# Optimization experiments

Measured on AMD Instinct MI355X. Metric: run time of the kernel, lower is better.

Reference implementation:

```python
import jax, jax.numpy as jnp
import numpy as np
from jax import lax

B, PH, PW, D = 4, 256, 256, 128
WS, SS, NG, NH = 8, 4, 2, 4
HID = int(D * 2.0)
DC = D // 2  # ngram-context channel dim


def _window_partition(x, ws):
    b, h, w, c = x.shape
    x = x.reshape(b, h // ws, ws, w // ws, ws, c).transpose(0, 1, 3, 2, 4, 5)
    return x.reshape(-1, ws, ws, c), (h // ws, w // ws)


def _window_unpartition(win, nwin):
    wh, ww = nwin
    _, s1, s2, c = win.shape
    x = win.reshape(-1, wh, ww, s1, s2, c).transpose(0, 1, 3, 2, 4, 5)
    return x.reshape(-1, wh * s1, ww * s2, c)


def _rel_pos_index(wh, ww):
    coords = np.stack(np.meshgrid(np.arange(wh), np.arange(ww), indexing='ij')).reshape(2, -1)
    rel = (coords[:, :, None] - coords[:, None, :]).transpose(1, 2, 0)
    rel[:, :, 0] += wh - 1
    rel[:, :, 1] += ww - 1
    rel[:, :, 0] *= 2 * ww - 1
    return rel.sum(-1)  # [N, N]

RPI_MAIN = jnp.asarray(_rel_pos_index(WS, WS))
RPI_NG = jnp.asarray(_rel_pos_index(NG, NG))


def _layernorm(x, g, b, eps=1e-5):
    mu = x.mean(-1, keepdims=True)
    var = ((x - mu) ** 2).mean(-1, keepdims=True)
    return (x - mu) * lax.rsqrt(var + eps) * g + b


def _mhsa(x, qkv_w, qkv_b, proj_w, proj_b, bias_table, rpi, nheads, mask=None):
    b_, n, c = x.shape
    hd = c // nheads
    qkv = (x @ qkv_w.T + qkv_b).reshape(b_, n, 3, nheads, hd).transpose(2, 0, 3, 1, 4)
    q, k, v = qkv[0] * (hd ** -0.5), qkv[1], qkv[2]
    attn = jnp.einsum('bhnd,bhmd->bhnm', q, k) + bias_table[rpi].transpose(2, 0, 1)[None]
    if mask is not None:
        nw = mask.shape[0]
        attn = (attn.reshape(b_ // nw, nw, nheads, n, n) + mask[None, :, None]).reshape(b_, nheads, n, n)
    attn = jax.nn.softmax(attn, axis=-1)
    out = jnp.einsum('bhnm,bhmd->bhnd', attn, v).transpose(0, 2, 1, 3).reshape(b_, n, c)
    return out @ proj_w.T + proj_b


def _make_mask(ph, pw):
    img = np.zeros((ph, pw), np.float32)
    cnt = 0
    for h in (slice(0, -WS), slice(-WS, -SS), slice(-SS, None)):
        for w in (slice(0, -WS), slice(-WS, -SS), slice(-SS, None)):
            img[h, w] = cnt
            cnt += 1
    mw, _ = _window_partition(jnp.asarray(img)[None, :, :, None], WS)
    mw = mw.reshape(-1, WS * WS)
    diff = mw[:, None, :] - mw[:, :, None]
    return jnp.where(diff != 0, -100.0, 0.0)  # [wh*ww, WS*WS, WS*WS]


def _seq_refl_pad(u, back):
    # sequential reflective window pad by ngram-1 on H and W (front if back else end)
    nh, nw = u.shape[2], u.shape[3]
    if back:
        ih = np.concatenate([np.arange(1, NG), np.arange(nh)])
        iw = np.concatenate([np.arange(1, NG), np.arange(nw)])
    else:
        ih = np.concatenate([np.arange(nh), np.arange(nh - NG, nh - 1)])
        iw = np.concatenate([np.arange(nw), np.arange(nw - NG, nw - 1)])
    return u[:, :, ih][:, :, :, iw]


def _sliding_attn(u, ng_qkv_w, ng_qkv_b, ng_proj_w, ng_proj_b, ng_bias, wh, ww):
    # u: [B, DC, wh+NG-1, ww+NG-1]  (padded unigram)
    hi = (np.arange(wh)[:, None] + np.arange(NG)[None, :]).reshape(-1)
    wi = (np.arange(ww)[:, None] + np.arange(NG)[None, :]).reshape(-1)
    slide = u[:, :, hi][:, :, :, wi].transpose(0, 2, 3, 1)  # [B, wh*NG, ww*NG, DC]
    win, nwin = _window_partition(slide, NG)
    win = win.reshape(-1, NG * NG, DC)
    ctx = _mhsa(win, ng_qkv_w, ng_qkv_b, ng_proj_w, ng_proj_b, ng_bias, RPI_NG, NH)
    ctx = _window_unpartition(ctx.reshape(-1, NG, NG, DC), nwin)  # [B, wh*NG, ww*NG, DC]
    ctx = ctx.transpose(0, 3, 1, 2)
    b = ctx.shape[0]
    return ctx.reshape(b, DC, wh, NG, ww, NG).mean(axis=(3, 5))  # AvgPool2d(NG) -> [B, DC, wh, ww]


def reference(x, uni_w, uni_b, ng_qkv_w, ng_qkv_b, ng_proj_w, ng_proj_b, ng_bias,
              merge_w, merge_b, qkv_w, qkv_b, proj_w, proj_b, bias_table,
              n1_g, n1_b, n2_g, n2_b, fc1_w, fc1_b, fc2_w, fc2_b, ph, pw):
    b = x.shape[0]
    xi = x.reshape(b, ph, pw, D)
    wh, ww = ph // WS, pw // WS
    # --- NGram context ---
    xc = xi.transpose(0, 3, 1, 2)  # NCHW
    uni = lax.conv_general_dilated(xc, uni_w, (WS, WS), 'VALID', feature_group_count=DC,
                                   dimension_numbers=('NCHW', 'OIHW', 'NCHW'))
    uni = uni + uni_b[None, :, None, None]  # [B, DC, wh, ww]
    ctx_f = _sliding_attn(_seq_refl_pad(uni, False), ng_qkv_w, ng_qkv_b, ng_proj_w, ng_proj_b, ng_bias, wh, ww)
    ctx_b = _sliding_attn(_seq_refl_pad(uni, True), ng_qkv_w, ng_qkv_b, ng_proj_w, ng_proj_b, ng_bias, wh, ww)
    ctx = jnp.concatenate([ctx_f, ctx_b], axis=1)  # [B, D, wh, ww]
    ctx = jnp.einsum('bchw,oc->bohw', ctx, merge_w) + merge_b[None, :, None, None]  # 1x1 merge conv
    ctx = ctx.transpose(0, 2, 3, 1)  # [B, wh, ww, D]
    # --- inject context into semi-partitioned windows ---
    windows = xi.reshape(b, wh, WS, ww, WS, D).transpose(0, 1, 3, 2, 4, 5)  # [B, wh, ww, WS, WS, D]
    windows = windows + ctx[:, :, :, None, None, :]
    xw = windows.transpose(0, 1, 3, 2, 4, 5).reshape(b, ph, pw, D)
    # --- cyclic shift + masked window attention ---
    xw = jnp.roll(xw, (-SS, -SS), axis=(1, 2))
    win, _ = _window_partition(xw, WS)
    win = win.reshape(-1, WS * WS, D)
    mask = _make_mask(ph, pw)
    aw = _mhsa(win, qkv_w, qkv_b, proj_w, proj_b, bias_table, RPI_MAIN, NH, mask=mask)
    shifted = _window_unpartition(aw.reshape(-1, WS, WS, D), (wh, ww))  # [B, ph, pw, D]
    rev = jnp.roll(shifted, (SS, SS), axis=(1, 2)).reshape(b, ph * pw, D)
    # --- residual + post-branch layernorm, then FFN ---
    x1 = x + _layernorm(rev, n1_g, n1_b)
    h = jax.nn.gelu(x1 @ fc1_w.T + fc1_b, approximate=False)
    ffn = h @ fc2_w.T + fc2_b
    return x1 + _layernorm(ffn, n2_g, n2_b)


def setup_inputs() -> dict:
    key = jax.random.key(0)
    ks = jax.random.split(key, 12)
    w = lambda k, shape: jax.random.normal(k, shape, jnp.float32) * 0.02
    return {
        'x': jax.random.normal(ks[0], (B, PH * PW, D), jnp.float32),
        'uni_w': w(ks[1], (DC, 2, WS, WS)),
        'uni_b': jnp.zeros((DC,), jnp.float32),
        'ng_qkv_w': w(ks[2], (3 * DC, DC)),
        'ng_qkv_b': jnp.zeros((3 * DC,), jnp.float32),
        'ng_proj_w': w(ks[3], (DC, DC)),
        'ng_proj_b': jnp.zeros((DC,), jnp.float32),
        'ng_bias': w(ks[4], ((2 * NG - 1) ** 2, NH)),
        'merge_w': w(ks[5], (D, D)),
        'merge_b': jnp.zeros((D,), jnp.float32),
        'qkv_w': w(ks[6], (3 * D, D)),
        'qkv_b': jnp.zeros((3 * D,), jnp.float32),
        'proj_w': w(ks[7], (D, D)),
        'proj_b': jnp.zeros((D,), jnp.float32),
        'bias_table': w(ks[8], ((2 * WS - 1) ** 2, NH)),
        'n1_g': jnp.ones((D,), jnp.float32),
        'n1_b': jnp.zeros((D,), jnp.float32),
        'n2_g': jnp.ones((D,), jnp.float32),
        'n2_b': jnp.zeros((D,), jnp.float32),
        'fc1_w': w(ks[9], (HID, D)),
        'fc1_b': jnp.zeros((HID,), jnp.float32),
        'fc2_w': w(ks[10], (D, HID)),
        'fc2_b': jnp.zeros((D,), jnp.float32),
        'ph': PH,
        'pw': PW,
    }
```

## Files before the change

### kernel.cpp

```cpp
#include <hip/hip_runtime.h>

typedef __bf16 bf16x8 __attribute__((ext_vector_type(8)));
typedef __bf16 bf16x4 __attribute__((ext_vector_type(4)));
typedef float  f32x4  __attribute__((ext_vector_type(4)));

#define QSCALE 0.17677669529663687f
#define XF_LD 132

__device__ __forceinline__ f32x4 mfma16(bf16x8 a, bf16x8 b, f32x4 c) {
  return __builtin_amdgcn_mfma_f32_16x16x32_bf16(a, b, c, 0, 0, 0);
}

__device__ __forceinline__ int swz_idx(int row, int col, int rowChunks) {
  return row * (rowChunks << 3) + ((((col >> 3) ^ (row & 7)) << 3) | (col & 7));
}

__device__ __forceinline__ bf16x8 ld_tile(const __bf16* t, int rowChunks,
                                          int rowBase, int chunkBase, int lane) {
  int row = rowBase + (lane & 15);
  int c = (chunkBase + (lane >> 4)) ^ (row & 7);
  return *(const bf16x8*)(t + row * (rowChunks << 3) + (c << 3));
}

__device__ __forceinline__ bf16x8 ld_pack(const __bf16* pk, int nt, int ks,
                                          int ksteps, int lane) {
  int idx = ((nt * ksteps + ks) * 64 + lane) * 8;
  return *(const bf16x8*)(pk + idx);
}

__global__ void k_prep(const float* __restrict__ qkvw, const float* __restrict__ projw,
                       const float* __restrict__ fc1w, const float* __restrict__ fc2w,
                       const float* __restrict__ ngqkvw,
                       const float* __restrict__ ngprojw, const float* __restrict__ ngprojb,
                       const float* __restrict__ mergew, const float* __restrict__ mergeb,
                       const float* __restrict__ bt,
                       const float* __restrict__ x, const float* __restrict__ uw,
                       const float* __restrict__ ub,
                       __bf16* __restrict__ pk, float* __restrict__ w12T,
                       float* __restrict__ fb, float* __restrict__ btf,
                       float* __restrict__ qkvTg, float* __restrict__ uni) {
  int blk = blockIdx.x;
  if (blk < 2048) {
    int bidx = blk * 2 + (threadIdx.x >> 7);
    int b = bidx >> 10, oh = (bidx >> 5) & 31, ow = bidx & 31;
    int d = threadIdx.x & 127;
    const float* xb = x + (((size_t)((b << 16) + ((oh << 3) << 8) + (ow << 3))) << 7) + d;
    const float* w = uw + d * 64;
    float acc = 0.f;
#pragma unroll
    for (int kh = 0; kh < 8; ++kh)
#pragma unroll
      for (int kw = 0; kw < 8; ++kw)
        acc += xb[(size_t)(((kh << 8) + kw)) << 7] * w[kh * 8 + kw];
    acc += __shfl_xor(acc, 1);
    if (!(d & 1)) uni[((size_t)bidx << 6) + (d >> 1)] = acc + ub[d >> 1];
  } else if (blk < 2560) {
    int i = (blk - 2048) * 256 + threadIdx.x;
    const float* src; int K; int e; int scaleQ = 0;
    if (i < 32768)      { src = qkvw;             K = 128; e = i;          scaleQ = 1; }
    else if (i < 49152) { src = qkvw + 256 * 128; K = 128; e = i - 32768; }
    else if (i < 65536) { src = projw;            K = 128; e = i - 49152; }
    else if (i < 98304) { src = fc1w;             K = 128; e = i - 65536; }
    else                { src = fc2w;             K = 256; e = i - 98304; }
    int i8 = e & 7, ln = (e >> 3) & 63, t = e >> 9;
    int ls = (K == 256) ? 3 : 2;
    int ks = t & ((1 << ls) - 1), nt = t >> ls;
    int row = (nt << 4) + (ln & 15);
    int k = (ks << 5) + ((ln >> 4) << 3) + i8;
    float v = src[row * K + k];
    if (scaleQ && row < 128) v *= QSCALE;
    pk[i] = (__bf16)v;
  } else if (blk < 2816) {
    int idx = (blk - 2560) * 256 + threadIdx.x;
    int v = idx >> 14, h = (idx >> 12) & 3, kk = (idx >> 6) & 63, q = idx & 63;
    int s1n = q >> 3, s2n = q & 7, s1m = kk >> 3, s2m = kk & 7;
    int rpi = (s1n - s1m + 7) * 15 + (s2n - s2m + 7);
    float val = bt[rpi * 4 + h];
    if (((v & 1) && ((s1n < 4) != (s1m < 4))) ||
        ((v & 2) && ((s2n < 4) != (s2m < 4))))
      val -= 100.f;
    btf[idx] = val;
  } else if (blk < 2864) {
    int idx = (blk - 2816) * 256 + threadIdx.x;
    int c = idx / 192, o = idx - c * 192;
    qkvTg[idx] = ngqkvw[o * 64 + c] * (o < 64 ? 0.25f : 1.f);
  } else {
    int idx = (blk - 2864) * 256 + threadIdx.x;
    if (idx < 16384) {
      int which = idx >> 13;
      int r = idx & 8191;
      int e = r >> 7, o = r & 127;
      float a = 0.f;
#pragma unroll 8
      for (int d = 0; d < 64; ++d)
        a += mergew[o * 128 + which * 64 + d] * ngprojw[d * 64 + e];
      w12T[idx] = a;
    } else if (idx < 16384 + 128) {
      int o = idx - 16384;
      float a = mergeb[o];
#pragma unroll 8
      for (int d = 0; d < 64; ++d)
        a += (mergew[o * 128 + d] + mergew[o * 128 + 64 + d]) * ngprojb[d];
      fb[o] = a;
    }
  }
}

__global__ void __launch_bounds__(256)
k_ngram(const float* __restrict__ uni, const float* __restrict__ qkvTg,
        const float* __restrict__ ngqkvb, const float* __restrict__ ngbias,
        const float* __restrict__ w12T, const float* __restrict__ fbg,
        float* __restrict__ ctx) {
  extern __shared__ float sm[];
  float* tokl = sm;
  float* qs   = tokl + 2304;
  float* prs  = qs + 6912;
  float* avgl = prs + 256;
  float* ngb  = avgl + 1024;
  float* fbs  = ngb + 192;
  float* nbias= fbs + 128;

  const int t = threadIdx.x;
  const int bidx = blockIdx.x;
  const int b = bidx >> 7, ii = (bidx >> 2) & 31, jq = bidx & 3;
  const int j0 = jq * 8;

  if (t < 192) ngb[t] = ngqkvb[t] * (t < 64 ? 0.25f : 1.f);
  if (t < 128) fbs[t] = fbg[t];
  if (t < 36)  nbias[t] = ngbias[t];
  {
    int w = t >> 6, lane = t & 63;
    int dir = w >> 1, rr = w & 1;
    int pi = ii + rr;
    int srcr = (dir == 0) ? ((pi < 32) ? pi : 30) : ((pi == 0) ? 1 : pi - 1);
#pragma unroll
    for (int cc = 0; cc < 9; ++cc) {
      int pj = j0 + cc;
      int srcc = (dir == 0) ? ((pj < 32) ? pj : 30) : ((pj == 0) ? 1 : pj - 1);
      tokl[((dir * 2 + rr) * 9 + cc) * 64 + lane] =
          uni[(size_t)((b * 32 + srcr) * 32 + srcc) * 64 + lane];
    }
  }
  __syncthreads();

  {
    int w = t >> 6, lane = t & 63;
    for (int itp = 0; itp < 9; ++itp) {
      int pos = itp * 4 + w;
      const float* tk = tokl + pos * 64;
      float a0 = ngb[lane], a1 = ngb[64 + lane], a2 = ngb[128 + lane];
#pragma unroll 4
      for (int c = 0; c < 64; ++c) {
        float tv = tk[c];
        const float* qr = qkvTg + c * 192;
        a0 += qr[lane] * tv;
        a1 += qr[64 + lane] * tv;
        a2 += qr[128 + lane] * tv;
      }
      float* dst = qs + pos * 192;
      dst[lane] = a0; dst[64 + lane] = a1; dst[128 + lane] = a2;
    }
  }
  __syncthreads();

  {
    int dw = t >> 4;
    int idx = t & 15, h = idx >> 2, p = idx & 3;
    int dir = dw >> 3, jl = dw & 7;
    const float* qp = qs + ((dir * 2 + (p >> 1)) * 9 + jl + (p & 1)) * 192 + h * 16;
    float s[4];
#pragma unroll
    for (int m = 0; m < 4; ++m) {
      const float* km = qs + ((dir * 2 + (m >> 1)) * 9 + jl + (m & 1)) * 192 + 64 + h * 16;
      float a = 0.f;
#pragma unroll
      for (int e = 0; e < 16; ++e) a += qp[e] * km[e];
      int bi2 = ((p >> 1) - (m >> 1) + 1) * 3 + ((p & 1) - (m & 1) + 1);
      s[m] = a + nbias[bi2 * 4 + h];
    }
    float mx = fmaxf(fmaxf(s[0], s[1]), fmaxf(s[2], s[3]));
    float e0 = __expf(s[0] - mx), e1 = __expf(s[1] - mx);
    float e2 = __expf(s[2] - mx), e3 = __expf(s[3] - mx);
    float inv = 1.f / (e0 + e1 + e2 + e3);
    float p0 = e0 * inv, p1 = e1 * inv, p2 = e2 * inv, p3 = e3 * inv;
    p0 += __shfl_xor(p0, 1); p0 += __shfl_xor(p0, 2);
    p1 += __shfl_xor(p1, 1); p1 += __shfl_xor(p1, 2);
    p2 += __shfl_xor(p2, 1); p2 += __shfl_xor(p2, 2);
    p3 += __shfl_xor(p3, 1); p3 += __shfl_xor(p3, 2);
    if (p == 0) {
      float* d = prs + (dw * 4 + h) * 4;
      d[0] = p0; d[1] = p1; d[2] = p2; d[3] = p3;
    }
  }
  __syncthreads();

  {
    int w = t >> 6, lane = t & 63;
#pragma unroll
    for (int it = 0; it < 4; ++it) {
      int dw = it * 4 + w;
      int dir = dw >> 3, jl = dw & 7;
      int h = lane >> 4;
      float a = 0.f;
#pragma unroll
      for (int m = 0; m < 4; ++m) {
        float pm = prs[(dw * 4 + h) * 4 + m];
        float vv = qs[((dir * 2 + (m >> 1)) * 9 + jl + (m & 1)) * 192 + 128 + lane];
        a += pm * vv;
      }
      avgl[dw * 64 + lane] = a * 0.25f;
    }
  }
  __syncthreads();

  {
#pragma unroll
    for (int it = 0; it < 4; ++it) {
      int id = it * 256 + t;
      int win = id >> 7, o = id & 127;
      const float* af = avgl + win * 64;
      const float* ab = avgl + (8 + win) * 64;
      float a = fbs[o];
#pragma unroll 4
      for (int c = 0; c < 64; ++c)
        a += w12T[c * 128 + o] * af[c] + w12T[8192 + c * 128 + o] * ab[c];
      int j = j0 + win;
      ctx[((size_t)((b * 32 + ii) * 32 + j)) * 128 + o] = a;
    }
  }
}

__global__ void __launch_bounds__(1024, 2)
k_main(const float* __restrict__ xin, const float* __restrict__ ctx,
       const __bf16* __restrict__ pk_qkv, const __bf16* __restrict__ pk_wv,
       const __bf16* __restrict__ pk_proj, const __bf16* __restrict__ pk_fc1,
       const __bf16* __restrict__ pk_fc2,
       const float* __restrict__ qkvb, const float* __restrict__ projb,
       const float* __restrict__ btf,
       const float* __restrict__ n1g, const float* __restrict__ n1b,
       const float* __restrict__ n2g, const float* __restrict__ n2b,
       const float* __restrict__ fc1b, const float* __restrict__ fc2b,
       float* __restrict__ outp) {
  extern __shared__ char smem[];
  __bf16* Xbf = (__bf16*)smem;
  __bf16* QO  = (__bf16*)(smem + 16 * 1024);
  __bf16* Kl  = (__bf16*)(smem + 32 * 1024);
  __bf16* Vt  = (__bf16*)(smem + 48 * 1024);
  __bf16* Pl  = (__bf16*)(smem + 64 * 1024);
  float*  Rf  = (float*)(smem + 48 * 1024);
  __bf16* Hl  = (__bf16*)(smem + 16 * 1024);
  float*  Ff  = (float*)(smem + 48 * 1024);

  const int widx = blockIdx.x;
  const int b = widx >> 10, wi = (widx >> 5) & 31, wj = widx & 31;
  const int tid = threadIdx.x;
  const int lane = tid & 63, wv = tid >> 6;
  const int lm = lane & 15, lg = lane >> 4;

  float xsv[8];
  float xr[8];

  {
    int n = tid >> 4, c = tid & 15;
    int ts1 = n >> 3, ts2 = n & 7;
    int hh = ((wi << 3) + ts1 + 4) & 255;
    int ww = ((wj << 3) + ts2 + 4) & 255;
    const float* xp = xin + (((size_t)((b << 16) + (hh << 8) + ww)) << 7);
    const float* cp = ctx + (((size_t)((((b << 5) + (hh >> 3)) << 5) + (ww >> 3))) << 7);
    int d0 = c << 2, d1 = 64 + (c << 2);
    float4 x0 = *(const float4*)(xp + d0);
    float4 x1 = *(const float4*)(xp + d1);
    float4 c0 = *(const float4*)(cp + d0);
    float4 c1 = *(const float4*)(cp + d1);
    xsv[0] = x0.x; xsv[1] = x0.y; xsv[2] = x0.z; xsv[3] = x0.w;
    xsv[4] = x1.x; xsv[5] = x1.y; xsv[6] = x1.z; xsv[7] = x1.w;
    bf16x4 pa, pb;
    pa[0] = (__bf16)(x0.x + c0.x); pa[1] = (__bf16)(x0.y + c0.y);
    pa[2] = (__bf16)(x0.z + c0.z); pa[3] = (__bf16)(x0.w + c0.w);
    pb[0] = (__bf16)(x1.x + c1.x); pb[1] = (__bf16)(x1.y + c1.y);
    pb[2] = (__bf16)(x1.z + c1.z); pb[3] = (__bf16)(x1.w + c1.w);
    int cA = d0 >> 3, oA = d0 & 7;
    int cB = d1 >> 3, oB = d1 & 7;
    *(bf16x4*)(Xbf + (n << 7) + (((cA ^ (n & 7)) << 3) | oA)) = pa;
    *(bf16x4*)(Xbf + (n << 7) + (((cB ^ (n & 7)) << 3) | oB)) = pb;
  }
  __syncthreads();

  {
    int ntG = wv;
    bf16x8 wf[4];
#pragma unroll
    for (int ks = 0; ks < 4; ++ks) wf[ks] = ld_pack(pk_qkv, ntG, ks, 4, lane);
    int col0 = (ntG << 4) + (lg << 2);
    float bias[4];
#pragma unroll
    for (int r = 0; r < 4; ++r)
      bias[r] = (ntG < 8) ? qkvb[col0 + r] * QSCALE : qkvb[col0 + r];
    __bf16* dst = (ntG < 8) ? QO : Kl;
    int cc0 = col0 & 127;
    for (int nt = 0; nt < 4; ++nt) {
      bf16x8 xf[4];
#pragma unroll
      for (int ks = 0; ks < 4; ++ks) xf[ks] = ld_tile(Xbf, 16, nt * 16, ks * 4, lane);
      f32x4 acc = {0.f, 0.f, 0.f, 0.f};
#pragma unroll
      for (int ks = 0; ks < 4; ++ks) acc = mfma16(wf[ks], xf[ks], acc);
      int tok = nt * 16 + lm;
      bf16x4 p4;
#pragma unroll
      for (int r = 0; r < 4; ++r) p4[r] = (__bf16)(acc[r] + bias[r]);
      *(bf16x4*)(dst + (tok << 7) + ((((cc0 >> 3) ^ (tok & 7)) << 3) | (cc0 & 7))) = p4;
    }
  }
  {
    int mtG = wv >> 1;
    bf16x8 wvf[4];
#pragma unroll
    for (int ks = 0; ks < 4; ++ks) wvf[ks] = ld_pack(pk_wv, mtG, ks, 4, lane);
    int ch = (mtG << 4) + lm;
    float vb = qkvb[256 + ch];
#pragma unroll
    for (int mt2 = 0; mt2 < 2; ++mt2) {
      int mt = ((wv & 1) << 1) + mt2;
      bf16x8 xf[4];
#pragma unroll
      for (int ks = 0; ks < 4; ++ks) xf[ks] = ld_tile(Xbf, 16, mt * 16, ks * 4, lane);
      f32x4 acc = {0.f, 0.f, 0.f, 0.f};
#pragma unroll
      for (int ks = 0; ks < 4; ++ks) acc = mfma16(xf[ks], wvf[ks], acc);
      int tok0 = mt * 16 + (lg << 2);
      bf16x4 p4;
#pragma unroll
      for (int r = 0; r < 4; ++r) p4[r] = (__bf16)(acc[r] + vb);
      *(bf16x4*)(Vt + (ch << 6) + ((((tok0 >> 3) ^ (ch & 7)) << 3) | (tok0 & 7))) = p4;
    }
  }
  __syncthreads();

  const int h = wv >> 2, mq = wv & 3;
  __bf16* Pme = Pl + (h << 12);
  {
    bf16x8 aq = ld_tile(QO, 16, mq * 16, h * 4, lane);
    bf16x8 bk[4];
#pragma unroll
    for (int nt = 0; nt < 4; ++nt)
      bk[nt] = ld_tile(Kl, 16, nt * 16, h * 4, lane);
    f32x4 sc[4];
#pragma unroll
    for (int nt = 0; nt < 4; ++nt) {
      f32x4 z = {0.f, 0.f, 0.f, 0.f};
      sc[nt] = mfma16(bk[nt], aq, z);
    }
    const int variant = (wi == 31 ? 1 : 0) | (wj == 31 ? 2 : 0);
    const float* btw = btf + (((variant << 2) + h) << 12);
    const int q = mq * 16 + lm;
    float v[4][4];
    float ssum = 0.f;
#pragma unroll
    for (int nt = 0; nt < 4; ++nt)
#pragma unroll
      for (int r = 0; r < 4; ++r) {
        int kk = nt * 16 + (lg << 2) + r;
        float e = __expf(sc[nt][r] + btw[(kk << 6) + q]);
        v[nt][r] = e;
        ssum += e;
      }
    ssum += __shfl_xor(ssum, 16);
    ssum += __shfl_xor(ssum, 32);
    float rinv = 1.f / ssum;
#pragma unroll
    for (int nt = 0; nt < 4; ++nt) {
      bf16x4 p4;
#pragma unroll
      for (int r = 0; r < 4; ++r) p4[r] = (__bf16)(v[nt][r] * rinv);
      int k0 = nt * 16 + (lg << 2);
      *(bf16x4*)(Pme + (q << 6) + ((((k0 >> 3) ^ (q & 7)) << 3) | (k0 & 7))) = p4;
    }
  }

  {
    bf16x8 ap[2];
#pragma unroll
    for (int ks = 0; ks < 2; ++ks)
      ap[ks] = ld_tile(Pme, 8, mq * 16, ks * 4, lane);
#pragma unroll
    for (int nt = 0; nt < 2; ++nt) {
      bf16x8 bv0 = ld_tile(Vt, 8, h * 32 + nt * 16, 0, lane);
      bf16x8 bv1 = ld_tile(Vt, 8, h * 32 + nt * 16, 4, lane);
      f32x4 acc = {0.f, 0.f, 0.f, 0.f};
      acc = mfma16(bv0, ap[0], acc);
      acc = mfma16(bv1, ap[1], acc);
      int q = mq * 16 + lm;
      int ch0 = h * 32 + nt * 16 + (lg << 2);
      bf16x4 p4;
#pragma unroll
      for (int r = 0; r < 4; ++r) p4[r] = (__bf16)acc[r];
      *(bf16x4*)(QO + (q << 7) + ((((ch0 >> 3) ^ (q & 7)) << 3) | (ch0 & 7))) = p4;
    }
  }
  __syncthreads();

  {
    int ntG = wv >> 1;
    int ch0 = (ntG << 4) + (lg << 2);
    float pb[4];
#pragma unroll
    for (int r = 0; r < 4; ++r) pb[r] = projb[ch0 + r];
    bf16x8 wf[4];
#pragma unroll
    for (int ks = 0; ks < 4; ++ks) wf[ks] = ld_pack(pk_proj, ntG, ks, 4, lane);
#pragma unroll
    for (int mt2 = 0; mt2 < 2; ++mt2) {
      int mt = ((wv & 1) << 1) + mt2;
      f32x4 acc = {0.f, 0.f, 0.f, 0.f};
#pragma unroll
      for (int ks = 0; ks < 4; ++ks)
        acc = mfma16(wf[ks], ld_tile(QO, 16, mt * 16, ks * 4, lane), acc);
      int tok = mt * 16 + lm;
      float4 st;
      st.x = acc[0] + pb[0]; st.y = acc[1] + pb[1];
      st.z = acc[2] + pb[2]; st.w = acc[3] + pb[3];
      *(float4*)(Rf + tok * XF_LD + ch0) = st;
    }
  }
  __syncthreads();

  {
    int n = tid >> 4, c = tid & 15;
    int d0 = c << 2, d1 = 64 + (c << 2);
    const float* rrow = Rf + n * XF_LD;
    float4 r0 = *(const float4*)(rrow + d0);
    float4 r1 = *(const float4*)(rrow + d1);
    float sum1 = r0.x + r0.y + r0.z + r0.w + r1.x + r1.y + r1.z + r1.w;
    float sum2 = r0.x * r0.x + r0.y * r0.y + r0.z * r0.z + r0.w * r0.w
               + r1.x * r1.x + r1.y * r1.y + r1.z * r1.z + r1.w * r1.w;
    sum1 += __shfl_xor(sum1, 1); sum1 += __shfl_xor(sum1, 2);
    sum1 += __shfl_xor(sum1, 4); sum1 += __shfl_xor(sum1, 8);
    sum2 += __shfl_xor(sum2, 1); sum2 += __shfl_xor(sum2, 2);
    sum2 += __shfl_xor(sum2, 4); sum2 += __shfl_xor(sum2, 8);
    float mean = sum1 * 0.0078125f;
    float var = sum2 * 0.0078125f - mean * mean;
    float rstd = rsqrtf(var + 1e-5f);
    float rv[8] = {r0.x, r0.y, r0.z, r0.w, r1.x, r1.y, r1.z, r1.w};
    bf16x4 pa, pb;
#pragma unroll
    for (int e = 0; e < 4; ++e) {
      float x1 = xsv[e] + (rv[e] - mean) * rstd * n1g[d0 + e] + n1b[d0 + e];
      xr[e] = x1; pa[e] = (__bf16)x1;
    }
#pragma unroll
    for (int e = 0; e < 4; ++e) {
      float x1 = xsv[4 + e] + (rv[4 + e] - mean) * rstd * n1g[d1 + e] + n1b[d1 + e];
      xr[4 + e] = x1; pb[e] = (__bf16)x1;
    }
    int cA = d0 >> 3, oA = d0 & 7;
    int cB = d1 >> 3, oB = d1 & 7;
    *(bf16x4*)(Xbf + (n << 7) + (((cA ^ (n & 7)) << 3) | oA)) = pa;
    *(bf16x4*)(Xbf + (n << 7) + (((cB ^ (n & 7)) << 3) | oB)) = pb;
  }
  __syncthreads();

  {
    int ntG = wv;
    int ch0 = (ntG << 4) + (lg << 2);
    float b1[4];
#pragma unroll
    for (int r = 0; r < 4; ++r) b1[r] = fc1b[ch0 + r];
    bf16x8 wf[4];
#pragma unroll
    for (int ks = 0; ks < 4; ++ks) wf[ks] = ld_pack(pk_fc1, ntG, ks, 4, lane);
    for (int nt = 0; nt < 4; ++nt) {
      f32x4 acc = {0.f, 0.f, 0.f, 0.f};
#pragma unroll
      for (int ks = 0; ks < 4; ++ks)
        acc = mfma16(wf[ks], ld_tile(Xbf, 16, nt * 16, ks * 4, lane), acc);
      int tok = nt * 16 + lm;
      bf16x4 p4;
#pragma unroll
      for (int r = 0; r < 4; ++r) {
        float hv = acc[r] + b1[r];
        float u = hv * (0.7978845608f + 0.0356774081f * hv * hv);
        float e = __expf(2.f * u);
        hv = hv - hv / (e + 1.f);
        p4[r] = (__bf16)hv;
      }
      *(bf16x4*)(Hl + (tok << 8) + ((((ch0 >> 3) ^ (tok & 7)) << 3) | (ch0 & 7))) = p4;
    }
  }
  __syncthreads();

  {
    int ntG = wv >> 1;
    int ch0 = (ntG << 4) + (lg << 2);
    float b2[4];
#pragma unroll
    for (int r = 0; r < 4; ++r) b2[r] = fc2b[ch0 + r];
    bf16x8 wf[8];
#pragma unroll
    for (int ks = 0; ks < 8; ++ks) wf[ks] = ld_pack(pk_fc2, ntG, ks, 8, lane);
#pragma unroll
    for (int mt2 = 0; mt2 < 2; ++mt2) {
      int mt = ((wv & 1) << 1) + mt2;
      f32x4 acc = {0.f, 0.f, 0.f, 0.f};
#pragma unroll
      for (int ks = 0; ks < 8; ++ks)
        acc = mfma16(wf[ks], ld_tile(Hl, 32, mt * 16, ks * 4, lane), acc);
      int tok = mt * 16 + lm;
      float4 st;
      st.x = acc[0] + b2[0]; st.y = acc[1] + b2[1];
      st.z = acc[2] + b2[2]; st.w = acc[3] + b2[3];
      *(float4*)(Ff + tok * XF_LD + ch0) = st;
    }
  }
  __syncthreads();

  {
    int n = tid >> 4, c = tid & 15;
    int d0 = c << 2, d1 = 64 + (c << 2);
    const float* frow = Ff + n * XF_LD;
    float4 f0 = *(const float4*)(frow + d0);
    float4 f1 = *(const float4*)(frow + d1);
    float sum1 = f0.x + f0.y + f0.z + f0.w + f1.x + f1.y + f1.z + f1.w;
    float sum2 = f0.x * f0.x + f0.y * f0.y + f0.z * f0.z + f0.w * f0.w
               + f1.x * f1.x + f1.y * f1.y + f1.z * f1.z + f1.w * f1.w;
    sum1 += __shfl_xor(sum1, 1); sum1 += __shfl_xor(sum1, 2);
    sum1 += __shfl_xor(sum1, 4); sum1 += __shfl_xor(sum1, 8);
    sum2 += __shfl_xor(sum2, 1); sum2 += __shfl_xor(sum2, 2);
    sum2 += __shfl_xor(sum2, 4); sum2 += __shfl_xor(sum2, 8);
    float mean = sum1 * 0.0078125f;
    float var = sum2 * 0.0078125f - mean * mean;
    float rstd = rsqrtf(var + 1e-5f);
    int ts1 = n >> 3, ts2 = n & 7;
    int hh = ((wi << 3) + ts1 + 4) & 255;
    int ww = ((wj << 3) + ts2 + 4) & 255;
    float* op = outp + (((size_t)((b << 16) + (hh << 8) + ww)) << 7);
    float fv[8] = {f0.x, f0.y, f0.z, f0.w, f1.x, f1.y, f1.z, f1.w};
    float4 o0, o1;
    o0.x = xr[0] + (fv[0] - mean) * rstd * n2g[d0 + 0] + n2b[d0 + 0];
    o0.y = xr[1] + (fv[1] - mean) * rstd * n2g[d0 + 1] + n2b[d0 + 1];
    o0.z = xr[2] + (fv[2] - mean) * rstd * n2g[d0 + 2] + n2b[d0 + 2];
    o0.w = xr[3] + (fv[3] - mean) * rstd * n2g[d0 + 3] + n2b[d0 + 3];
    o1.x = xr[4] + (fv[4] - mean) * rstd * n2g[d1 + 0] + n2b[d1 + 0];
    o1.y = xr[5] + (fv[5] - mean) * rstd * n2g[d1 + 1] + n2b[d1 + 1];
    o1.z = xr[6] + (fv[6] - mean) * rstd * n2g[d1 + 2] + n2b[d1 + 2];
    o1.w = xr[7] + (fv[7] - mean) * rstd * n2g[d1 + 3] + n2b[d1 + 3];
    *(float4*)(op + d0) = o0;
    *(float4*)(op + d1) = o1;
  }
}

extern "C" void kernel_launch(void* const* d_in, const int* in_sizes, int n_in,
                              void* d_out, int out_size, void* d_ws, size_t ws_size,
                              hipStream_t stream) {
  const float* x      = (const float*)d_in[0];
  const float* uni_w  = (const float*)d_in[1];
  const float* uni_b  = (const float*)d_in[2];
  const float* ngqkvw = (const float*)d_in[3];
  const float* ngqkvb = (const float*)d_in[4];
  const float* ngprojw= (const float*)d_in[5];
  const float* ngprojb= (const float*)d_in[6];
  const float* ngbias = (const float*)d_in[7];
  const float* mergew = (const float*)d_in[8];
  const float* mergeb = (const float*)d_in[9];
  const float* qkvw   = (const float*)d_in[10];
  const float* qkvb   = (const float*)d_in[11];
  const float* projw  = (const float*)d_in[12];
  const float* projb  = (const float*)d_in[13];
  const float* bt     = (const float*)d_in[14];
  const float* n1g    = (const float*)d_in[15];
  const float* n1b    = (const float*)d_in[16];
  const float* n2g    = (const float*)d_in[17];
  const float* n2b    = (const float*)d_in[18];
  const float* fc1w   = (const float*)d_in[19];
  const float* fc1b   = (const float*)d_in[20];
  const float* fc2w   = (const float*)d_in[21];
  const float* fc2b   = (const float*)d_in[22];

  char* ws = (char*)d_ws;
  float*  uni = (float*)ws;
  float*  ctx = (float*)(ws + (1 << 20));
  __bf16* pk  = (__bf16*)(ws + (3 << 20));
  __bf16* pk_qkv  = pk;
  __bf16* pk_wv   = pk + 32768;
  __bf16* pk_proj = pk + 49152;
  __bf16* pk_fc1  = pk + 65536;
  __bf16* pk_fc2  = pk + 98304;
  float*  w12T = (float*)(ws + (7 << 19));
  float*  fb   = w12T + 16384;
  float*  btf  = (float*)(ws + 3840 * 1024);
  float*  qkvTg= (float*)(ws + 4096 * 1024);

  k_prep<<<2929, 256, 0, stream>>>(qkvw, projw, fc1w, fc2w, ngqkvw, ngprojw, ngprojb,
                                   mergew, mergeb, bt, x, uni_w, uni_b,
                                   pk, w12T, fb, btf, qkvTg, uni);
  k_ngram<<<512, 256, 43408, stream>>>(uni, qkvTg, ngqkvb, ngbias, w12T, fb, ctx);
  k_main<<<4096, 1024, 98304, stream>>>(x, ctx, pk_qkv, pk_wv, pk_proj, pk_fc1, pk_fc2,
                                        qkvb, projb, btf, n1g, n1b, n2g, n2b, fc1b, fc2b,
                                        (float*)d_out);
}
```

Measured before the change: 269.4 us.

## Use 32x32x16 MFMA tiles for QKV and FC1 projections in main kernel

Replaces the 16x16x32 MFMA loops for the Q/K projection and the FC1 layer with 32x32x16 MFMA tiles. Each wave now computes a 32-channel by 32-token block over eight k-steps. The prep kernel gains extra blocks that pack the QKV and FC1 weights into the fragment layout the 32x32 instruction expects. The goal is fewer LDS fragment reads and fewer MFMA issues per output, paid for with 16-register accumulators and a larger prep launch.

```diff
diff --git a/kernel.cpp b/kernel.cpp
--- a/kernel.cpp
+++ b/kernel.cpp
@@ -3,12 +3,16 @@
 typedef __bf16 bf16x8 __attribute__((ext_vector_type(8)));
 typedef __bf16 bf16x4 __attribute__((ext_vector_type(4)));
 typedef float  f32x4  __attribute__((ext_vector_type(4)));
+typedef float  f32x16 __attribute__((ext_vector_type(16)));
 
 #define QSCALE 0.17677669529663687f
 #define XF_LD 132
 
 __device__ __forceinline__ f32x4 mfma16(bf16x8 a, bf16x8 b, f32x4 c) {
   return __builtin_amdgcn_mfma_f32_16x16x32_bf16(a, b, c, 0, 0, 0);
+}
+__device__ __forceinline__ f32x16 mfma32(bf16x8 a, bf16x8 b, f32x16 c) {
+  return __builtin_amdgcn_mfma_f32_32x32x16_bf16(a, b, c, 0, 0, 0);
 }
 
 __device__ __forceinline__ int swz_idx(int row, int col, int rowChunks) {
@@ -22,10 +26,21 @@
   return *(const bf16x8*)(t + row * (rowChunks << 3) + (c << 3));
 }
 
+__device__ __forceinline__ bf16x8 ld_tile32(const __bf16* t, int rowChunks,
+                                            int rowBase, int ks16, int lane) {
+  int row = rowBase + (lane & 31);
+  int c = ((ks16 << 1) + (lane >> 5)) ^ (row & 7);
+  return *(const bf16x8*)(t + row * (rowChunks << 3) + (c << 3));
+}
+
 __device__ __forceinline__ bf16x8 ld_pack(const __bf16* pk, int nt, int ks,
                                           int ksteps, int lane) {
   int idx = ((nt * ksteps + ks) * 64 + lane) * 8;
   return *(const bf16x8*)(pk + idx);
+}
+__device__ __forceinline__ bf16x8 ld_pack32(const __bf16* pk2, int nt32, int ks16,
+                                            int lane) {
+  return *(const bf16x8*)(pk2 + ((((nt32 << 3) + ks16) << 6) + lane) * 8);
 }
 
 __global__ void k_prep(const float* __restrict__ qkvw, const float* __restrict__ projw,
@@ -38,7 +53,8 @@
                        const float* __restrict__ ub,
                        __bf16* __restrict__ pk, float* __restrict__ w12T,
                        float* __restrict__ fb, float* __restrict__ btf,
-                       float* __restrict__ qkvTg, float* __restrict__ uni) {
+                       float* __restrict__ qkvTg, __bf16* __restrict__ pk2,
+                       float* __restrict__ uni) {
   int blk = blockIdx.x;
   if (blk < 2048) {
     int bidx = blk * 2 + (threadIdx.x >> 7);
@@ -84,7 +100,7 @@
     int idx = (blk - 2816) * 256 + threadIdx.x;
     int c = idx / 192, o = idx - c * 192;
     qkvTg[idx] = ngqkvw[o * 64 + c] * (o < 64 ? 0.25f : 1.f);
-  } else {
+  } else if (blk < 2929) {
     int idx = (blk - 2864) * 256 + threadIdx.x;
     if (idx < 16384) {
       int which = idx >> 13;
@@ -103,6 +119,19 @@
         a += (mergew[o * 128 + d] + mergew[o * 128 + 64 + d]) * ngprojb[d];
       fb[o] = a;
     }
+  } else {
+    int e = (blk - 2929) * 256 + threadIdx.x;
+    int i8 = e & 7, ln = (e >> 3) & 63, t2 = e >> 9;
+    int ks = t2 & 7, nt = (t2 >> 3) & 7;
+    int ch = (nt << 5) + (ln & 31);
+    int k = (ks << 4) + ((ln >> 5) << 3) + i8;
+    if (e < 32768) {
+      float v = qkvw[ch * 128 + k];
+      if (ch < 128) v *= QSCALE;
+      pk2[e] = (__bf16)v;
+    } else {
+      pk2[e] = (__bf16)fc1w[ch * 128 + k];
+    }
   }
 }
 
@@ -232,9 +261,9 @@
 
 __global__ void __launch_bounds__(1024, 2)
 k_main(const float* __restrict__ xin, const float* __restrict__ ctx,
-       const __bf16* __restrict__ pk_qkv, const __bf16* __restrict__ pk_wv,
-       const __bf16* __restrict__ pk_proj, const __bf16* __restrict__ pk_fc1,
-       const __bf16* __restrict__ pk_fc2,
+       const __bf16* __restrict__ pk2_qkv, const __bf16* __restrict__ pk2_fc1,
+       const __bf16* __restrict__ pk_wv,
+       const __bf16* __restrict__ pk_proj, const __bf16* __restrict__ pk_fc2,
        const float* __restrict__ qkvb, const float* __restrict__ projb,
        const float* __restrict__ btf,
        const float* __restrict__ n1g, const float* __restrict__ n1b,
@@ -287,28 +316,28 @@
   __syncthreads();
 
   {
-    int ntG = wv;
-    bf16x8 wf[4];
-#pragma unroll
-    for (int ks = 0; ks < 4; ++ks) wf[ks] = ld_pack(pk_qkv, ntG, ks, 4, lane);
-    int col0 = (ntG << 4) + (lg << 2);
-    float bias[4];
-#pragma unroll
-    for (int r = 0; r < 4; ++r)
-      bias[r] = (ntG < 8) ? qkvb[col0 + r] * QSCALE : qkvb[col0 + r];
-    __bf16* dst = (ntG < 8) ? QO : Kl;
-    int cc0 = col0 & 127;
-    for (int nt = 0; nt < 4; ++nt) {
-      bf16x8 xf[4];
-#pragma unroll
-      for (int ks = 0; ks < 4; ++ks) xf[ks] = ld_tile(Xbf, 16, nt * 16, ks * 4, lane);
-      f32x4 acc = {0.f, 0.f, 0.f, 0.f};
-#pragma unroll
-      for (int ks = 0; ks < 4; ++ks) acc = mfma16(wf[ks], xf[ks], acc);
-      int tok = nt * 16 + lm;
+    int nt32 = wv & 7, th = wv >> 3;
+    int chBase = nt32 << 5, tokBase = th << 5;
+    f32x16 acc = {};
+#pragma unroll
+    for (int ks = 0; ks < 8; ++ks)
+      acc = mfma32(ld_pack32(pk2_qkv, nt32, ks, lane),
+                   ld_tile32(Xbf, 16, tokBase, ks, lane), acc);
+    int tok = tokBase + (lane & 31);
+    int hi = lane >> 5;
+    const bool isQ = (nt32 < 4);
+    __bf16* dst = isQ ? QO : Kl;
+    float s = isQ ? QSCALE : 1.f;
+#pragma unroll
+    for (int g = 0; g < 4; ++g) {
+      int ch0 = chBase + (g << 3) + (hi << 2);
+      float4 bb = *(const float4*)(qkvb + ch0);
+      int cc0 = ch0 & 127;
       bf16x4 p4;
-#pragma unroll
-      for (int r = 0; r < 4; ++r) p4[r] = (__bf16)(acc[r] + bias[r]);
+      p4[0] = (__bf16)(acc[(g << 2) + 0] + bb.x * s);
+      p4[1] = (__bf16)(acc[(g << 2) + 1] + bb.y * s);
+      p4[2] = (__bf16)(acc[(g << 2) + 2] + bb.z * s);
+      p4[3] = (__bf16)(acc[(g << 2) + 3] + bb.w * s);
       *(bf16x4*)(dst + (tok << 7) + ((((cc0 >> 3) ^ (tok & 7)) << 3) | (cc0 & 7))) = p4;
     }
   }
@@ -461,24 +490,24 @@
   __syncthreads();
 
   {
-    int ntG = wv;
-    int ch0 = (ntG << 4) + (lg << 2);
-    float b1[4];
-#pragma unroll
-    for (int r = 0; r < 4; ++r) b1[r] = fc1b[ch0 + r];
-    bf16x8 wf[4];
-#pragma unroll
-    for (int ks = 0; ks < 4; ++ks) wf[ks] = ld_pack(pk_fc1, ntG, ks, 4, lane);
-    for (int nt = 0; nt < 4; ++nt) {
-      f32x4 acc = {0.f, 0.f, 0.f, 0.f};
-#pragma unroll
-      for (int ks = 0; ks < 4; ++ks)
-        acc = mfma16(wf[ks], ld_tile(Xbf, 16, nt * 16, ks * 4, lane), acc);
-      int tok = nt * 16 + lm;
+    int nt32 = wv & 7, th = wv >> 3;
+    int chBase = nt32 << 5, tokBase = th << 5;
+    f32x16 acc = {};
+#pragma unroll
+    for (int ks = 0; ks < 8; ++ks)
+      acc = mfma32(ld_pack32(pk2_fc1, nt32, ks, lane),
+                   ld_tile32(Xbf, 16, tokBase, ks, lane), acc);
+    int tok = tokBase + (lane & 31);
+    int hi = lane >> 5;
+#pragma unroll
+    for (int g = 0; g < 4; ++g) {
+      int ch0 = chBase + (g << 3) + (hi << 2);
+      float4 bb = *(const float4*)(fc1b + ch0);
+      float bv[4] = {bb.x, bb.y, bb.z, bb.w};
       bf16x4 p4;
 #pragma unroll
       for (int r = 0; r < 4; ++r) {
-        float hv = acc[r] + b1[r];
+        float hv = acc[(g << 2) + r] + bv[r];
         float u = hv * (0.7978845608f + 0.0356774081f * hv * hv);
         float e = __expf(2.f * u);
         hv = hv - hv / (e + 1.f);
@@ -580,21 +609,22 @@
   float*  uni = (float*)ws;
   float*  ctx = (float*)(ws + (1 << 20));
   __bf16* pk  = (__bf16*)(ws + (3 << 20));
-  __bf16* pk_qkv  = pk;
   __bf16* pk_wv   = pk + 32768;
   __bf16* pk_proj = pk + 49152;
-  __bf16* pk_fc1  = pk + 65536;
   __bf16* pk_fc2  = pk + 98304;
   float*  w12T = (float*)(ws + (7 << 19));
   float*  fb   = w12T + 16384;
   float*  btf  = (float*)(ws + 3840 * 1024);
   float*  qkvTg= (float*)(ws + 4096 * 1024);
-
-  k_prep<<<2929, 256, 0, stream>>>(qkvw, projw, fc1w, fc2w, ngqkvw, ngprojw, ngprojb,
+  __bf16* pk2  = (__bf16*)(ws + 4160 * 1024);
+  __bf16* pk2_qkv = pk2;
+  __bf16* pk2_fc1 = pk2 + 32768;
+
+  k_prep<<<3185, 256, 0, stream>>>(qkvw, projw, fc1w, fc2w, ngqkvw, ngprojw, ngprojb,
                                    mergew, mergeb, bt, x, uni_w, uni_b,
-                                   pk, w12T, fb, btf, qkvTg, uni);
+                                   pk, w12T, fb, btf, qkvTg, pk2, uni);
   k_ngram<<<512, 256, 43408, stream>>>(uni, qkvTg, ngqkvb, ngbias, w12T, fb, ctx);
-  k_main<<<4096, 1024, 98304, stream>>>(x, ctx, pk_qkv, pk_wv, pk_proj, pk_fc1, pk_fc2,
+  k_main<<<4096, 1024, 98304, stream>>>(x, ctx, pk2_qkv, pk2_fc1, pk_wv, pk_proj, pk_fc2,
                                         qkvb, projb, btf, n1g, n1b, n2g, n2b, fc1b, fc2b,
                                         (float*)d_out);
 }
```

Measured after the change: 280.7 us. 1.04x slower.
